# Kernel optimization log

Hardware: AMD Instinct MI355X
Metric: run time of the kernel (lower is better)

The kernel has to match this reference:

```python
import jax, jax.numpy as jnp
import numpy as np

B, N, C, H, E = 16, 512, 128, 8, 131072
Nn = B * N
Dh = C // H
EPS = 1e-5


def setup_inputs() -> dict:
    key = jax.random.key(0)
    ks = jax.random.split(key, 16)
    s = C ** -0.5
    x = jax.random.normal(ks[0], (Nn, C), dtype=jnp.float32)
    edge_index = jax.random.randint(ks[1], (2, E), 0, Nn)
    batch = jnp.arange(Nn) // N  # B equal-sized graphs, sorted
    attn_bias = jax.random.normal(ks[2], (B, N, N, H), dtype=jnp.float32)
    return {
        "x": x,
        "edge_index": edge_index,
        "batch": batch,
        "attn_bias": attn_bias,
        "conv_w": jax.random.normal(ks[3], (C, C)) * s,
        "conv_b": jnp.zeros((C,)),
        "wq": jax.random.normal(ks[4], (C, C)) * s,
        "bq": jnp.zeros((C,)),
        "wk": jax.random.normal(ks[5], (C, C)) * s,
        "bk": jnp.zeros((C,)),
        "wv": jax.random.normal(ks[6], (C, C)) * s,
        "bv": jnp.zeros((C,)),
        "wo": jax.random.normal(ks[7], (C, C)) * s,
        "bo": jnp.zeros((C,)),
        "w1": jax.random.normal(ks[8], (C, 2 * C)) * s,
        "b1": jnp.zeros((2 * C,)),
        "w2": jax.random.normal(ks[9], (2 * C, C)) * (2 * C) ** -0.5,
        "b2": jnp.zeros((C,)),
        "g1": jnp.ones((C,)), "be1": jnp.zeros((C,)),
        "g2": jnp.ones((C,)), "be2": jnp.zeros((C,)),
        "g3": jnp.ones((C,)), "be3": jnp.zeros((C,)),
    }


def _bn(h, g, b):
    # BatchNorm1d over the node dimension (training-mode batch statistics)
    mu = h.mean(axis=0)
    var = h.var(axis=0)  # biased, matches torch normalization
    return g * (h - mu) * jax.lax.rsqrt(var + EPS) + b


def reference(x, edge_index, batch, attn_bias,
              conv_w, conv_b, wq, bq, wk, bk, wv, bv, wo, bo,
              w1, b1, w2, b2, g1, be1, g2, be2, g3, be3):
    n_nodes, ch = x.shape
    bsz, n_max, _, heads = attn_bias.shape
    dh = ch // heads

    # ---- GCN conv (self loops + symmetric norm) -> dropout(0) + residual + norm1
    loops = jnp.arange(n_nodes)
    src = jnp.concatenate([edge_index[0], loops])
    dst = jnp.concatenate([edge_index[1], loops])
    deg = jax.ops.segment_sum(jnp.ones_like(src, dtype=x.dtype), dst, num_segments=n_nodes)
    dinv = jax.lax.rsqrt(jnp.maximum(deg, 1.0))
    xw = x @ conv_w
    msg = xw[src] * (dinv[src] * dinv[dst])[:, None]
    hconv = jax.ops.segment_sum(msg, dst, num_segments=n_nodes) + conv_b
    h1 = _bn(hconv + x, g1, be1)

    # ---- dense batch (equal-sized sorted graphs -> pure reshape, mask all-valid)
    xd = x.reshape(bsz, n_max, ch)
    q = ((xd @ wq + bq) * (dh ** -0.5)).reshape(bsz, n_max, heads, dh)
    k = (xd @ wk + bk).reshape(bsz, n_max, heads, dh)
    v = (xd @ wv + bv).reshape(bsz, n_max, heads, dh)
    scores = jnp.einsum('bqhd,bkhd->bqkh', q, k) + attn_bias  # [B,N,N,H]
    probs = jax.nn.softmax(scores, axis=2)
    att = jnp.einsum('bqkh,bkhd->bqhd', probs, v).reshape(bsz, n_max, ch)
    att = att @ wo + bo
    h2 = _bn(att.reshape(n_nodes, ch) + x, g2, be2)

    # ---- combine branches, MLP with residual, norm3
    out = h1 + h2
    mlp = jax.nn.relu(out @ w1 + b1) @ w2 + b2
    return _bn(out + mlp, g3, be3)
```

## Files before the change

### kernel.cpp

```cpp
#include <hip/hip_runtime.h>
#include <cstddef>

#define NN 8192
#define CC 128

static __device__ inline unsigned f2bf_pack(float a, float b) {
  unsigned ua = __builtin_bit_cast(unsigned, a);
  ua += 0x7fffu + ((ua >> 16) & 1u);
  unsigned ub = __builtin_bit_cast(unsigned, b);
  ub += 0x7fffu + ((ub >> 16) & 1u);
  return (ua >> 16) | (ub & 0xffff0000u);
}
static __device__ inline float bf_lo(unsigned u) { return __builtin_bit_cast(float, u << 16); }
static __device__ inline float bf_hi(unsigned u) { return __builtin_bit_cast(float, u & 0xffff0000u); }

typedef const __attribute__((address_space(1))) void gvoid_t;
typedef __attribute__((address_space(3))) void lvoid_t;
static __device__ inline void glds16(const float* g, float* l) {
  __builtin_amdgcn_global_load_lds((gvoid_t*)g, (lvoid_t*)l, 16, 0, 0);
}


__global__ __launch_bounds__(256) void count_deg_int_k(const int* __restrict__ dst, int* degi, int E) {
  int i = blockIdx.x * 256 + threadIdx.x;
  if (i < E) atomicAdd(&degi[dst[i]], 1);
}

__global__ __launch_bounds__(256) void dinv_k(const int* __restrict__ degi, float* __restrict__ dinv, int n) {
  int i = blockIdx.x * 256 + threadIdx.x;
  if (i < n) dinv[i] = rsqrtf((float)(degi[i] + 1));
}

__global__ __launch_bounds__(256) void scan_k(const int* __restrict__ degi, int* __restrict__ rowstart,
                                              int* __restrict__ cursor) {
  __shared__ int partial[256];
  int t = threadIdx.x;
  int base = t * 32;
  int local[32];
  int s = 0;
#pragma unroll
  for (int i = 0; i < 32; ++i) { local[i] = s; s += degi[base + i]; }
  partial[t] = s;
  __syncthreads();
  for (int off = 1; off < 256; off <<= 1) {
    int v = (t >= off) ? partial[t - off] : 0;
    __syncthreads();
    partial[t] += v;
    __syncthreads();
  }
  int offset = partial[t] - s;
#pragma unroll
  for (int i = 0; i < 32; ++i) {
    rowstart[base + i] = offset + local[i];
    cursor[base + i] = offset + local[i];
  }
  if (t == 255) rowstart[NN] = offset + s;
}

__global__ __launch_bounds__(256) void bucket_k(const int* __restrict__ src, const int* __restrict__ dst,
    int* __restrict__ cursor, int* __restrict__ col, int E) {
  int e = blockIdx.x * 256 + threadIdx.x;
  if (e >= E) return;
  int d = dst[e];
  int pos = atomicAdd(&cursor[d], 1);
  col[pos] = src[e];
}

__global__ __launch_bounds__(256) void gather_k(const int* __restrict__ rowstart, const int* __restrict__ col,
    const float* __restrict__ xws, const float* __restrict__ dinv, const float* __restrict__ cb,
    const float* __restrict__ x, float* __restrict__ h1) {
  int d = blockIdx.x * 2 + (threadIdx.x >> 7);
  int c = threadIdx.x & 127;
  int j0 = rowstart[d], j1 = rowstart[d + 1];
  float dd = dinv[d];
  float sum = 0.f;
  float v = 0.f;
  if (j0 < j1) v = xws[(size_t)col[j0] * CC + c];
  for (int j = j0; j < j1; ++j) {
    float v_next = 0.f;
    if (j + 1 < j1) v_next = xws[(size_t)col[j + 1] * CC + c];
    sum += v;
    v = v_next;
  }
  int idx = d * CC + c;
  sum += xws[idx];
  h1[idx] = sum * dd + cb[c] + x[idx];
}


__global__ __launch_bounds__(256) void bn_stats_k(const float* __restrict__ X,
    float* __restrict__ sums, float* __restrict__ sumsq) {
  int t = threadIdx.x;
  int c = t & 127, rg = t >> 7;
  int r0 = blockIdx.x * 64;
  float s = 0.f, sq = 0.f;
  for (int i = 0; i < 32; ++i) {
    float v = X[(size_t)(r0 + rg + 2 * i) * CC + c];
    s += v; sq += v * v;
  }
  atomicAdd(&sums[c], s);
  atomicAdd(&sumsq[c], sq);
}

__global__ __launch_bounds__(256) void combine_k(const float* __restrict__ h1, const float* __restrict__ h2,
    const float* __restrict__ st, const float* __restrict__ g1, const float* __restrict__ be1,
    const float* __restrict__ g2, const float* __restrict__ be2, float* __restrict__ out) {
  int idx = blockIdx.x * 256 + threadIdx.x;
  int c = idx & 127;
  float mu1 = st[c] * (1.f / NN);
  float var1 = st[128 + c] * (1.f / NN) - mu1 * mu1;
  float sc1 = g1[c] * rsqrtf(var1 + 1e-5f);
  float sh1 = be1[c] - mu1 * sc1;
  float mu2 = st[256 + c] * (1.f / NN);
  float var2 = st[384 + c] * (1.f / NN) - mu2 * mu2;
  float sc2 = g2[c] * rsqrtf(var2 + 1e-5f);
  float sh2 = be2[c] - mu2 * sc2;
  out[idx] = sc1 * h1[idx] + sh1 + sc2 * h2[idx] + sh2;
}

__global__ __launch_bounds__(256) void bn_apply_k(const float* __restrict__ h, const float* __restrict__ st,
    const float* __restrict__ g3, const float* __restrict__ be3, float* __restrict__ out) {
  int idx = blockIdx.x * 256 + threadIdx.x;
  int c = idx & 127;
  float mu = st[512 + c] * (1.f / NN);
  float var = st[640 + c] * (1.f / NN) - mu * mu;
  float sc = g3[c] * rsqrtf(var + 1e-5f);
  float sh = be3[c] - mu * sc;
  out[idx] = sc * h[idx] + sh;
}

__global__ __launch_bounds__(256) void gemm_k(const float* __restrict__ A, const float* __restrict__ W,
    const float* __restrict__ bias, const float* __restrict__ resid, const float* __restrict__ dscale,
    float* __restrict__ out, int M, int N, int K, float scale, int relu) {
  __shared__ float As[64 * 132];
  __shared__ float Ws[128 * 64];
  int t = threadIdx.x;
  int ty = t >> 4, tx = t & 15;
  int row0 = blockIdx.x * 64, n0 = blockIdx.y * 64;
  float acc[4][4] = {};
  for (int kc = 0; kc < K; kc += 128) {
#pragma unroll
    for (int j = 0; j < 8; ++j) {
      int f = t + 256 * j;
      int r = f >> 5, c4 = f & 31;
      *(float4*)(As + r * 132 + c4 * 4) = *(const float4*)(A + (size_t)(row0 + r) * K + kc + c4 * 4);
    }
#pragma unroll
    for (int j = 0; j < 8; ++j) {
      int f = t + 256 * j;
      int kr = f >> 4, c4 = f & 15;
      *(float4*)(Ws + kr * 64 + c4 * 4) = *(const float4*)(W + (size_t)(kc + kr) * N + n0 + c4 * 4);
    }
    __syncthreads();
    for (int k0 = 0; k0 < 128; k0 += 4) {
      float a[4][4], b[4][4];
#pragma unroll
      for (int i = 0; i < 4; ++i) {
        float4 t4 = *(const float4*)(As + (4 * ty + i) * 132 + k0);
        a[i][0] = t4.x; a[i][1] = t4.y; a[i][2] = t4.z; a[i][3] = t4.w;
      }
#pragma unroll
      for (int kk = 0; kk < 4; ++kk) {
        float4 t4 = *(const float4*)(Ws + (k0 + kk) * 64 + 4 * tx);
        b[kk][0] = t4.x; b[kk][1] = t4.y; b[kk][2] = t4.z; b[kk][3] = t4.w;
      }
#pragma unroll
      for (int kk = 0; kk < 4; ++kk)
#pragma unroll
        for (int i = 0; i < 4; ++i)
#pragma unroll
          for (int j = 0; j < 4; ++j)
            acc[i][j] += a[i][kk] * b[kk][j];
    }
    __syncthreads();
  }
  float4 bv = make_float4(0.f, 0.f, 0.f, 0.f);
  if (bias) bv = *(const float4*)(bias + n0 + 4 * tx);
#pragma unroll
  for (int i = 0; i < 4; ++i) {
    int row = row0 + 4 * ty + i;
    float ds = dscale ? dscale[row] : 1.f;
    float4 r;
    r.x = (acc[i][0] + bv.x) * scale * ds;
    r.y = (acc[i][1] + bv.y) * scale * ds;
    r.z = (acc[i][2] + bv.z) * scale * ds;
    r.w = (acc[i][3] + bv.w) * scale * ds;
    if (relu) { r.x = fmaxf(r.x, 0.f); r.y = fmaxf(r.y, 0.f); r.z = fmaxf(r.z, 0.f); r.w = fmaxf(r.w, 0.f); }
    size_t o = (size_t)row * N + n0 + 4 * tx;
    if (resid) {
      float4 rv = *(const float4*)(resid + o);
      r.x += rv.x; r.y += rv.y; r.z += rv.z; r.w += rv.w;
    }
    *(float4*)(out + o) = r;
  }
}

__global__ __launch_bounds__(64, 1) void attn_k(const float* __restrict__ Q, const float* __restrict__ K,
    const float* __restrict__ V, const float* __restrict__ bias,
    unsigned* __restrict__ pA, unsigned* __restrict__ pB, float* __restrict__ lbuf) {
  __shared__ float SM[2][4096];
  const int t = threadIdx.x;
  const int b = blockIdx.x >> 4;
  const int qt = blockIdx.x & 15;
  const int s = blockIdx.y;
  const int qq = t >> 3;
  const int h = t & 7;
  const int node_t = b * 512 + qt * 32;
  const int node0 = node_t + qq * 4;
  const int key0 = s * 128;
  const size_t kvb = ((size_t)b * 512 + key0) * CC;
  const float* bbase = bias + ((size_t)node_t * 512 + key0) * 8;

  float4 qf[4][4];
#pragma unroll
  for (int r = 0; r < 4; ++r)
#pragma unroll
    for (int j = 0; j < 4; ++j)
      qf[r][j] = *(const float4*)(Q + (size_t)(node0 + r) * CC + h * 16 + (((j + h) & 3) << 2));

  float4 acc[4][4];
  float l[4] = {0.f, 0.f, 0.f, 0.f};
#pragma unroll
  for (int r = 0; r < 4; ++r)
#pragma unroll
    for (int j = 0; j < 4; ++j) acc[r][j] = make_float4(0.f, 0.f, 0.f, 0.f);

  auto stage = [&](int ch, int bf) {
    const float* kg = K + kvb + ch * 1024;
    const float* vg = V + kvb + ch * 1024;
    float* ksl = &SM[bf][0];
    float* vsl = &SM[bf][1024];
    float* bsl = &SM[bf][2048];
#pragma unroll
    for (int i = 0; i < 4; ++i) {
      glds16(kg + i * 256 + t * 4, ksl + i * 256);
      glds16(vg + i * 256 + t * 4, vsl + i * 256);
    }
#pragma unroll
    for (int i = 0; i < 8; ++i) {
      int g = i * 64 + t;
      int q = g >> 4;
      int kkp = (g >> 1) & 7;
      int hq = g & 1;
      int kk = (kkp - (q >> 2)) & 7;
      glds16(bbase + (size_t)q * 4096 + (ch * 8 + kk) * 8 + hq * 4, bsl + i * 256);
    }
  };

  stage(0, 0);
  for (int ch = 0; ch < 16; ++ch) {
    int bf = ch & 1;
    if (ch + 1 < 16) stage(ch + 1, bf ^ 1);
    asm volatile("" ::: "memory");
    if (ch + 1 < 16) __builtin_amdgcn_s_waitcnt(0x4F70);
    else             __builtin_amdgcn_s_waitcnt(0x0F70);
    asm volatile("" ::: "memory");
    const float* ksl = &SM[bf][0];
    const float* vsl = &SM[bf][1024];
    const float* bsl = &SM[bf][2048];
#pragma unroll 2
    for (int kk = 0; kk < 8; ++kk) {
      float4 kr[4], vr[4];
#pragma unroll
      for (int j = 0; j < 4; ++j) {
        int off = kk * 128 + h * 16 + (((j + h) & 3) << 2);
        kr[j] = *(const float4*)(ksl + off);
        vr[j] = *(const float4*)(vsl + off);
      }
      int brot = ((kk + qq) & 7) << 3;
#pragma unroll
      for (int r = 0; r < 4; ++r) {
        float sc = bsl[(qq * 4 + r) * 64 + brot + h];
#pragma unroll
        for (int j = 0; j < 4; ++j)
          sc += qf[r][j].x * kr[j].x + qf[r][j].y * kr[j].y
              + qf[r][j].z * kr[j].z + qf[r][j].w * kr[j].w;
        float p = __expf(sc);
        l[r] += p;
#pragma unroll
        for (int j = 0; j < 4; ++j) {
          acc[r][j].x += p * vr[j].x; acc[r][j].y += p * vr[j].y;
          acc[r][j].z += p * vr[j].z; acc[r][j].w += p * vr[j].w;
        }
      }
    }
  }

  unsigned* pbase = (s < 2 ? pA : pB) + (size_t)(s & 1) * (NN * CC / 2);
#pragma unroll
  for (int r = 0; r < 4; ++r) {
    int slot = ((node0 + r) * 8 + h) * 8;
#pragma unroll
    for (int j = 0; j < 4; ++j) {
      int g = (j + h) & 3;
      unsigned u0 = f2bf_pack(acc[r][j].x, acc[r][j].y);
      unsigned u1 = f2bf_pack(acc[r][j].z, acc[r][j].w);
      *(uint2*)(pbase + slot + g * 2) = make_uint2(u0, u1);
    }
    lbuf[s * 65536 + (node0 + r) * 8 + h] = l[r];
  }
}

__global__ __launch_bounds__(256) void attn_merge_k(const unsigned* __restrict__ pA,
    const unsigned* __restrict__ pB, const float* __restrict__ lbuf, float* __restrict__ out) {
  int i = blockIdx.x * 256 + threadIdx.x;
  float L = lbuf[i] + lbuf[65536 + i] + lbuf[131072 + i] + lbuf[196608 + i];
  float inv = 1.f / L;
  float o[16];
#pragma unroll
  for (int d = 0; d < 16; ++d) o[d] = 0.f;
#pragma unroll
  for (int s = 0; s < 4; ++s) {
    const unsigned* pb = (s < 2 ? pA : pB) + (size_t)(s & 1) * (NN * CC / 2) + (size_t)i * 8;
    uint4 a = *(const uint4*)pb;
    uint4 b = *(const uint4*)(pb + 4);
    unsigned u[8] = {a.x, a.y, a.z, a.w, b.x, b.y, b.z, b.w};
#pragma unroll
    for (int j = 0; j < 8; ++j) {
      o[2*j]   += bf_lo(u[j]);
      o[2*j+1] += bf_hi(u[j]);
    }
  }
  float* po = out + (size_t)i * 16;
#pragma unroll
  for (int j = 0; j < 4; ++j)
    *(float4*)(po + 4 * j) = make_float4(o[4*j] * inv, o[4*j+1] * inv, o[4*j+2] * inv, o[4*j+3] * inv);
}


extern "C" void kernel_launch(void* const* d_in, const int* in_sizes, int n_in,
                              void* d_out, int out_size, void* d_ws, size_t ws_size,
                              hipStream_t stream) {
  const float* x      = (const float*)d_in[0];
  const int*   ei     = (const int*)d_in[1];
  const float* bias   = (const float*)d_in[3];
  const float* conv_w = (const float*)d_in[4];
  const float* conv_b = (const float*)d_in[5];
  const float* wq = (const float*)d_in[6];
  const float* bq = (const float*)d_in[7];
  const float* wk = (const float*)d_in[8];
  const float* bk = (const float*)d_in[9];
  const float* wv = (const float*)d_in[10];
  const float* bv = (const float*)d_in[11];
  const float* wo = (const float*)d_in[12];
  const float* bo = (const float*)d_in[13];
  const float* w1 = (const float*)d_in[14];
  const float* b1 = (const float*)d_in[15];
  const float* w2 = (const float*)d_in[16];
  const float* b2 = (const float*)d_in[17];
  const float* g1 = (const float*)d_in[18];
  const float* be1 = (const float*)d_in[19];
  const float* g2 = (const float*)d_in[20];
  const float* be2 = (const float*)d_in[21];
  const float* g3 = (const float*)d_in[22];
  const float* be3 = (const float*)d_in[23];
  int E = in_sizes[1] / 2;

  float* ws = (float*)d_ws;
  const size_t NC = (size_t)NN * CC;
  float* xw     = ws;
  float* h1pre  = ws + NC;
  float* qb     = ws + 2 * NC;
  float* kb     = ws + 3 * NC;
  float* vb     = ws + 4 * NC;
  float* h2pre  = ws + 5 * NC;
  float* outbuf = ws + 6 * NC;
  float* hid    = ws + 2 * NC;
  float* h3pre  = ws + 4 * NC;
  float* st     = ws + 7 * NC;
  float* dinv   = ws + 7 * NC + 768;
  int*   degi     = (int*)(ws + 7 * NC + 768 + NN);
  int*   rowstart = degi + NN;
  int*   cursor   = rowstart + NN + 1;
  int*   col      = cursor + NN;
  float* lbuf     = (float*)(col + E);

  hipMemsetAsync(degi, 0, NN * sizeof(int), stream);
  hipMemsetAsync(st, 0, 768 * sizeof(float), stream);

  count_deg_int_k<<<(E + 255) / 256, 256, 0, stream>>>(ei + E, degi, E);
  dinv_k<<<NN / 256, 256, 0, stream>>>(degi, dinv, NN);
  scan_k<<<1, 256, 0, stream>>>(degi, rowstart, cursor);
  bucket_k<<<(E + 255) / 256, 256, 0, stream>>>(ei, ei + E, cursor, col, E);
  gemm_k<<<dim3(NN / 64, 2), 256, 0, stream>>>(x, conv_w, nullptr, nullptr, dinv, xw, NN, CC, CC, 1.f, 0);
  gather_k<<<NN / 2, 256, 0, stream>>>(rowstart, col, xw, dinv, conv_b, x, h1pre);
  bn_stats_k<<<NN / 64, 256, 0, stream>>>(h1pre, st + 0, st + 128);

  gemm_k<<<dim3(NN / 64, 2), 256, 0, stream>>>(x, wq, bq, nullptr, nullptr, qb, NN, CC, CC, 0.25f, 0);
  gemm_k<<<dim3(NN / 64, 2), 256, 0, stream>>>(x, wk, bk, nullptr, nullptr, kb, NN, CC, CC, 1.f, 0);
  gemm_k<<<dim3(NN / 64, 2), 256, 0, stream>>>(x, wv, bv, nullptr, nullptr, vb, NN, CC, CC, 1.f, 0);
  attn_k<<<dim3(256, 4), 64, 0, stream>>>(qb, kb, vb, bias, (unsigned*)xw, (unsigned*)h2pre, lbuf);
  attn_merge_k<<<65536 / 256, 256, 0, stream>>>((unsigned*)xw, (unsigned*)h2pre, lbuf, outbuf);
  gemm_k<<<dim3(NN / 64, 2), 256, 0, stream>>>(outbuf, wo, bo, x, nullptr, h2pre, NN, CC, CC, 1.f, 0);
  bn_stats_k<<<NN / 64, 256, 0, stream>>>(h2pre, st + 256, st + 384);

  combine_k<<<NC / 256, 256, 0, stream>>>(h1pre, h2pre, st, g1, be1, g2, be2, outbuf);
  gemm_k<<<dim3(NN / 64, 4), 256, 0, stream>>>(outbuf, w1, b1, nullptr, nullptr, hid, NN, 2 * CC, CC, 1.f, 1);
  gemm_k<<<dim3(NN / 64, 2), 256, 0, stream>>>(hid, w2, b2, outbuf, nullptr, h3pre, NN, CC, 2 * CC, 1.f, 0);
  bn_stats_k<<<NN / 64, 256, 0, stream>>>(h3pre, st + 512, st + 640);
  bn_apply_k<<<NC / 256, 256, 0, stream>>>(h3pre, st, g3, be3, (float*)d_out);
}
```

Baseline: 440.7 us.

## Shrink attention blocks to one query row per thread for more occupancy

```diff
diff --git a/kernel.cpp b/kernel.cpp
--- a/kernel.cpp
+++ b/kernel.cpp
@@ -195,71 +195,66 @@
   }
 }
 
-__global__ __launch_bounds__(64, 1) void attn_k(const float* __restrict__ Q, const float* __restrict__ K,
+__global__ __launch_bounds__(64, 4) void attn_k(const float* __restrict__ Q, const float* __restrict__ K,
     const float* __restrict__ V, const float* __restrict__ bias,
     unsigned* __restrict__ pA, unsigned* __restrict__ pB, float* __restrict__ lbuf) {
-  __shared__ float SM[2][4096];
+  __shared__ float SM[2][1280];
   const int t = threadIdx.x;
-  const int b = blockIdx.x >> 4;
-  const int qt = blockIdx.x & 15;
-  const int s = blockIdx.y;
-  const int qq = t >> 3;
+  const int orig = blockIdx.x;
+  const int lb = ((orig & 7) << 9) | (orig >> 3);
+  const int grp = lb >> 6;
+  const int qt = lb & 63;
+  const int b = grp >> 2;
+  const int s = grp & 3;
+  const int q = t >> 3;
   const int h = t & 7;
-  const int node_t = b * 512 + qt * 32;
-  const int node0 = node_t + qq * 4;
+  const int node_t = b * 512 + qt * 8;
+  const int node = node_t + q;
   const int key0 = s * 128;
   const size_t kvb = ((size_t)b * 512 + key0) * CC;
   const float* bbase = bias + ((size_t)node_t * 512 + key0) * 8;
 
-  float4 qf[4][4];
-#pragma unroll
-  for (int r = 0; r < 4; ++r)
-#pragma unroll
-    for (int j = 0; j < 4; ++j)
-      qf[r][j] = *(const float4*)(Q + (size_t)(node0 + r) * CC + h * 16 + (((j + h) & 3) << 2));
-
-  float4 acc[4][4];
-  float l[4] = {0.f, 0.f, 0.f, 0.f};
-#pragma unroll
-  for (int r = 0; r < 4; ++r)
-#pragma unroll
-    for (int j = 0; j < 4; ++j) acc[r][j] = make_float4(0.f, 0.f, 0.f, 0.f);
+  float4 qf[4];
+#pragma unroll
+  for (int j = 0; j < 4; ++j)
+    qf[j] = *(const float4*)(Q + (size_t)node * CC + h * 16 + (((j + h) & 3) << 2));
+
+  float4 acc[4];
+  float lsum = 0.f;
+#pragma unroll
+  for (int j = 0; j < 4; ++j) acc[j] = make_float4(0.f, 0.f, 0.f, 0.f);
 
   auto stage = [&](int ch, int bf) {
-    const float* kg = K + kvb + ch * 1024;
-    const float* vg = V + kvb + ch * 1024;
+    const float* kg = K + kvb + ch * 512;
+    const float* vg = V + kvb + ch * 512;
     float* ksl = &SM[bf][0];
-    float* vsl = &SM[bf][1024];
-    float* bsl = &SM[bf][2048];
-#pragma unroll
-    for (int i = 0; i < 4; ++i) {
+    float* vsl = &SM[bf][512];
+    float* bsl = &SM[bf][1024];
+#pragma unroll
+    for (int i = 0; i < 2; ++i) {
       glds16(kg + i * 256 + t * 4, ksl + i * 256);
       glds16(vg + i * 256 + t * 4, vsl + i * 256);
     }
-#pragma unroll
-    for (int i = 0; i < 8; ++i) {
-      int g = i * 64 + t;
-      int q = g >> 4;
-      int kkp = (g >> 1) & 7;
-      int hq = g & 1;
-      int kk = (kkp - (q >> 2)) & 7;
-      glds16(bbase + (size_t)q * 4096 + (ch * 8 + kk) * 8 + hq * 4, bsl + i * 256);
+    {
+      int ql = t >> 3, kkp = (t >> 1) & 3, hq = t & 1;
+      int kks = (kkp - ql) & 3;
+      glds16(bbase + (size_t)ql * 4096 + (size_t)(ch * 4 + kks) * 8 + hq * 4, bsl);
     }
   };
 
   stage(0, 0);
-  for (int ch = 0; ch < 16; ++ch) {
+  for (int ch = 0; ch < 32; ++ch) {
     int bf = ch & 1;
-    if (ch + 1 < 16) stage(ch + 1, bf ^ 1);
+    if (ch + 1 < 32) stage(ch + 1, bf ^ 1);
     asm volatile("" ::: "memory");
-    if (ch + 1 < 16) __builtin_amdgcn_s_waitcnt(0x4F70);
+    if (ch + 1 < 32) __builtin_amdgcn_s_waitcnt(0x0F75);
     else             __builtin_amdgcn_s_waitcnt(0x0F70);
     asm volatile("" ::: "memory");
     const float* ksl = &SM[bf][0];
-    const float* vsl = &SM[bf][1024];
-    const float* bsl = &SM[bf][2048];
-#pragma unroll 2
-    for (int kk = 0; kk < 8; ++kk) {
+    const float* vsl = &SM[bf][512];
+    const float* bsl = &SM[bf][1024];
+#pragma unroll
+    for (int kk = 0; kk < 4; ++kk) {
       float4 kr[4], vr[4];
 #pragma unroll
       for (int j = 0; j < 4; ++j) {
@@ -267,38 +262,33 @@
         kr[j] = *(const float4*)(ksl + off);
         vr[j] = *(const float4*)(vsl + off);
       }
-      int brot = ((kk + qq) & 7) << 3;
-#pragma unroll
-      for (int r = 0; r < 4; ++r) {
-        float sc = bsl[(qq * 4 + r) * 64 + brot + h];
-#pragma unroll
-        for (int j = 0; j < 4; ++j)
-          sc += qf[r][j].x * kr[j].x + qf[r][j].y * kr[j].y
-              + qf[r][j].z * kr[j].z + qf[r][j].w * kr[j].w;
-        float p = __expf(sc);
-        l[r] += p;
-#pragma unroll
-        for (int j = 0; j < 4; ++j) {
-          acc[r][j].x += p * vr[j].x; acc[r][j].y += p * vr[j].y;
-          acc[r][j].z += p * vr[j].z; acc[r][j].w += p * vr[j].w;
-        }
+      float sc = bsl[q * 32 + (((kk + q) & 3) << 3) + h];
+#pragma unroll
+      for (int j = 0; j < 4; ++j)
+        sc += qf[j].x * kr[j].x + qf[j].y * kr[j].y
+            + qf[j].z * kr[j].z + qf[j].w * kr[j].w;
+      float p = __expf(sc);
+      lsum += p;
+#pragma unroll
+      for (int j = 0; j < 4; ++j) {
+        acc[j].x += p * vr[j].x; acc[j].y += p * vr[j].y;
+        acc[j].z += p * vr[j].z; acc[j].w += p * vr[j].w;
       }
     }
   }
 
   unsigned* pbase = (s < 2 ? pA : pB) + (size_t)(s & 1) * (NN * CC / 2);
-#pragma unroll
-  for (int r = 0; r < 4; ++r) {
-    int slot = ((node0 + r) * 8 + h) * 8;
-#pragma unroll
-    for (int j = 0; j < 4; ++j) {
-      int g = (j + h) & 3;
-      unsigned u0 = f2bf_pack(acc[r][j].x, acc[r][j].y);
-      unsigned u1 = f2bf_pack(acc[r][j].z, acc[r][j].w);
-      *(uint2*)(pbase + slot + g * 2) = make_uint2(u0, u1);
-    }
-    lbuf[s * 65536 + (node0 + r) * 8 + h] = l[r];
-  }
+  int slot = (node * 8 + h) * 8;
+  unsigned u[8];
+#pragma unroll
+  for (int g = 0; g < 4; ++g) {
+    int j = (g - h) & 3;
+    u[2 * g]     = f2bf_pack(acc[j].x, acc[j].y);
+    u[2 * g + 1] = f2bf_pack(acc[j].z, acc[j].w);
+  }
+  *(uint4*)(pbase + slot)     = make_uint4(u[0], u[1], u[2], u[3]);
+  *(uint4*)(pbase + slot + 4) = make_uint4(u[4], u[5], u[6], u[7]);
+  lbuf[s * 65536 + node * 8 + h] = lsum;
 }
 
 __global__ __launch_bounds__(256) void attn_merge_k(const unsigned* __restrict__ pA,
@@ -389,7 +379,7 @@
   gemm_k<<<dim3(NN / 64, 2), 256, 0, stream>>>(x, wq, bq, nullptr, nullptr, qb, NN, CC, CC, 0.25f, 0);
   gemm_k<<<dim3(NN / 64, 2), 256, 0, stream>>>(x, wk, bk, nullptr, nullptr, kb, NN, CC, CC, 1.f, 0);
   gemm_k<<<dim3(NN / 64, 2), 256, 0, stream>>>(x, wv, bv, nullptr, nullptr, vb, NN, CC, CC, 1.f, 0);
-  attn_k<<<dim3(256, 4), 64, 0, stream>>>(qb, kb, vb, bias, (unsigned*)xw, (unsigned*)h2pre, lbuf);
+  attn_k<<<4096, 64, 0, stream>>>(qb, kb, vb, bias, (unsigned*)xw, (unsigned*)h2pre, lbuf);
   attn_merge_k<<<65536 / 256, 256, 0, stream>>>((unsigned*)xw, (unsigned*)h2pre, lbuf, outbuf);
   gemm_k<<<dim3(NN / 64, 2), 256, 0, stream>>>(outbuf, wo, bo, x, nullptr, h2pre, NN, CC, CC, 1.f, 0);
   bn_stats_k<<<NN / 64, 256, 0, stream>>>(h2pre, st + 256, st + 384);
```

Result: no change. 446.2 us (+1.2%).

## Split attention keys into eight chunks and interleave query rows per thread

Applied to the files above, without the earlier changes.

```diff
diff --git a/kernel.cpp b/kernel.cpp
--- a/kernel.cpp
+++ b/kernel.cpp
@@ -195,19 +195,21 @@
   }
 }
 
-__global__ __launch_bounds__(64, 1) void attn_k(const float* __restrict__ Q, const float* __restrict__ K,
+__global__ __launch_bounds__(64, 2) void attn_k(const float* __restrict__ Q, const float* __restrict__ K,
     const float* __restrict__ V, const float* __restrict__ bias,
-    unsigned* __restrict__ pA, unsigned* __restrict__ pB, float* __restrict__ lbuf) {
-  __shared__ float SM[2][4096];
+    unsigned* __restrict__ p0, unsigned* __restrict__ p1,
+    unsigned* __restrict__ p2, unsigned* __restrict__ p3, float* __restrict__ lbuf) {
+  __shared__ float SM[2][2048];
   const int t = threadIdx.x;
-  const int b = blockIdx.x >> 4;
-  const int qt = blockIdx.x & 15;
-  const int s = blockIdx.y;
+  const int orig = blockIdx.x;
+  const int s = orig & 7;
+  const int qtg = orig >> 3;
+  const int b = qtg >> 4;
+  const int qt = qtg & 15;
   const int qq = t >> 3;
   const int h = t & 7;
   const int node_t = b * 512 + qt * 32;
-  const int node0 = node_t + qq * 4;
-  const int key0 = s * 128;
+  const int key0 = s * 64;
   const size_t kvb = ((size_t)b * 512 + key0) * CC;
   const float* bbase = bias + ((size_t)node_t * 512 + key0) * 8;
 
@@ -216,7 +218,7 @@
   for (int r = 0; r < 4; ++r)
 #pragma unroll
     for (int j = 0; j < 4; ++j)
-      qf[r][j] = *(const float4*)(Q + (size_t)(node0 + r) * CC + h * 16 + (((j + h) & 3) << 2));
+      qf[r][j] = *(const float4*)(Q + (size_t)(node_t + qq + 8 * r) * CC + h * 16 + (((j + h) & 3) << 2));
 
   float4 acc[4][4];
   float l[4] = {0.f, 0.f, 0.f, 0.f};
@@ -226,24 +228,23 @@
     for (int j = 0; j < 4; ++j) acc[r][j] = make_float4(0.f, 0.f, 0.f, 0.f);
 
   auto stage = [&](int ch, int bf) {
-    const float* kg = K + kvb + ch * 1024;
-    const float* vg = V + kvb + ch * 1024;
+    const float* kg = K + kvb + ch * 512;
+    const float* vg = V + kvb + ch * 512;
     float* ksl = &SM[bf][0];
-    float* vsl = &SM[bf][1024];
-    float* bsl = &SM[bf][2048];
-#pragma unroll
-    for (int i = 0; i < 4; ++i) {
+    float* vsl = &SM[bf][512];
+    float* bsl = &SM[bf][1024];
+#pragma unroll
+    for (int i = 0; i < 2; ++i) {
       glds16(kg + i * 256 + t * 4, ksl + i * 256);
       glds16(vg + i * 256 + t * 4, vsl + i * 256);
     }
 #pragma unroll
-    for (int i = 0; i < 8; ++i) {
-      int g = i * 64 + t;
-      int q = g >> 4;
-      int kkp = (g >> 1) & 7;
-      int hq = g & 1;
-      int kk = (kkp - (q >> 2)) & 7;
-      glds16(bbase + (size_t)q * 4096 + (ch * 8 + kk) * 8 + hq * 4, bsl + i * 256);
+    for (int i = 0; i < 4; ++i) {
+      int q = i * 8 + (t >> 3);
+      int kkp = (t >> 1) & 3;
+      int hq = t & 1;
+      int kks = (kkp - q) & 3;
+      glds16(bbase + (size_t)q * 4096 + (size_t)(ch * 4 + kks) * 8 + hq * 4, bsl + i * 256);
     }
   };
 
@@ -252,14 +253,14 @@
     int bf = ch & 1;
     if (ch + 1 < 16) stage(ch + 1, bf ^ 1);
     asm volatile("" ::: "memory");
-    if (ch + 1 < 16) __builtin_amdgcn_s_waitcnt(0x4F70);
+    if (ch + 1 < 16) __builtin_amdgcn_s_waitcnt(0x0F78);
     else             __builtin_amdgcn_s_waitcnt(0x0F70);
     asm volatile("" ::: "memory");
     const float* ksl = &SM[bf][0];
-    const float* vsl = &SM[bf][1024];
-    const float* bsl = &SM[bf][2048];
-#pragma unroll 2
-    for (int kk = 0; kk < 8; ++kk) {
+    const float* vsl = &SM[bf][512];
+    const float* bsl = &SM[bf][1024];
+#pragma unroll
+    for (int kk = 0; kk < 4; ++kk) {
       float4 kr[4], vr[4];
 #pragma unroll
       for (int j = 0; j < 4; ++j) {
@@ -267,10 +268,10 @@
         kr[j] = *(const float4*)(ksl + off);
         vr[j] = *(const float4*)(vsl + off);
       }
-      int brot = ((kk + qq) & 7) << 3;
+      int brot = ((kk + qq) & 3) << 3;
 #pragma unroll
       for (int r = 0; r < 4; ++r) {
-        float sc = bsl[(qq * 4 + r) * 64 + brot + h];
+        float sc = bsl[qq * 32 + r * 256 + brot + h];
 #pragma unroll
         for (int j = 0; j < 4; ++j)
           sc += qf[r][j].x * kr[j].x + qf[r][j].y * kr[j].y
@@ -286,32 +287,40 @@
     }
   }
 
-  unsigned* pbase = (s < 2 ? pA : pB) + (size_t)(s & 1) * (NN * CC / 2);
+  unsigned* preg = (s < 4) ? ((s < 2) ? p0 : p1) : ((s < 6) ? p2 : p3);
+  unsigned* pbase = preg + (size_t)(s & 1) * (NN * CC / 2);
 #pragma unroll
   for (int r = 0; r < 4; ++r) {
-    int slot = ((node0 + r) * 8 + h) * 8;
-#pragma unroll
-    for (int j = 0; j < 4; ++j) {
-      int g = (j + h) & 3;
-      unsigned u0 = f2bf_pack(acc[r][j].x, acc[r][j].y);
-      unsigned u1 = f2bf_pack(acc[r][j].z, acc[r][j].w);
-      *(uint2*)(pbase + slot + g * 2) = make_uint2(u0, u1);
-    }
-    lbuf[s * 65536 + (node0 + r) * 8 + h] = l[r];
-  }
-}
-
-__global__ __launch_bounds__(256) void attn_merge_k(const unsigned* __restrict__ pA,
-    const unsigned* __restrict__ pB, const float* __restrict__ lbuf, float* __restrict__ out) {
+    int node = node_t + qq + 8 * r;
+    int slot = (node * 8 + h) * 8;
+    unsigned u[8];
+#pragma unroll
+    for (int g = 0; g < 4; ++g) {
+      int j = (g - h) & 3;
+      u[2 * g]     = f2bf_pack(acc[r][j].x, acc[r][j].y);
+      u[2 * g + 1] = f2bf_pack(acc[r][j].z, acc[r][j].w);
+    }
+    *(uint4*)(pbase + slot)     = make_uint4(u[0], u[1], u[2], u[3]);
+    *(uint4*)(pbase + slot + 4) = make_uint4(u[4], u[5], u[6], u[7]);
+    lbuf[s * 65536 + node * 8 + h] = l[r];
+  }
+}
+
+__global__ __launch_bounds__(256) void attn_merge_k(const unsigned* __restrict__ p0,
+    const unsigned* __restrict__ p1, const unsigned* __restrict__ p2, const unsigned* __restrict__ p3,
+    const float* __restrict__ lbuf, float* __restrict__ out) {
   int i = blockIdx.x * 256 + threadIdx.x;
-  float L = lbuf[i] + lbuf[65536 + i] + lbuf[131072 + i] + lbuf[196608 + i];
+  float L = 0.f;
+#pragma unroll
+  for (int s = 0; s < 8; ++s) L += lbuf[s * 65536 + i];
   float inv = 1.f / L;
   float o[16];
 #pragma unroll
   for (int d = 0; d < 16; ++d) o[d] = 0.f;
-#pragma unroll
-  for (int s = 0; s < 4; ++s) {
-    const unsigned* pb = (s < 2 ? pA : pB) + (size_t)(s & 1) * (NN * CC / 2) + (size_t)i * 8;
+  const unsigned* regs[4] = {p0, p1, p2, p3};
+#pragma unroll
+  for (int s = 0; s < 8; ++s) {
+    const unsigned* pb = regs[s >> 1] + (size_t)(s & 1) * (NN * CC / 2) + (size_t)i * 8;
     uint4 a = *(const uint4*)pb;
     uint4 b = *(const uint4*)(pb + 4);
     unsigned u[8] = {a.x, a.y, a.z, a.w, b.x, b.y, b.z, b.w};
@@ -389,9 +398,11 @@
   gemm_k<<<dim3(NN / 64, 2), 256, 0, stream>>>(x, wq, bq, nullptr, nullptr, qb, NN, CC, CC, 0.25f, 0);
   gemm_k<<<dim3(NN / 64, 2), 256, 0, stream>>>(x, wk, bk, nullptr, nullptr, kb, NN, CC, CC, 1.f, 0);
   gemm_k<<<dim3(NN / 64, 2), 256, 0, stream>>>(x, wv, bv, nullptr, nullptr, vb, NN, CC, CC, 1.f, 0);
-  attn_k<<<dim3(256, 4), 64, 0, stream>>>(qb, kb, vb, bias, (unsigned*)xw, (unsigned*)h2pre, lbuf);
-  attn_merge_k<<<65536 / 256, 256, 0, stream>>>((unsigned*)xw, (unsigned*)h2pre, lbuf, outbuf);
-  gemm_k<<<dim3(NN / 64, 2), 256, 0, stream>>>(outbuf, wo, bo, x, nullptr, h2pre, NN, CC, CC, 1.f, 0);
+  attn_k<<<2048, 64, 0, stream>>>(qb, kb, vb, bias,
+      (unsigned*)xw, (unsigned*)h2pre, (unsigned*)d_out, (unsigned*)outbuf, lbuf);
+  attn_merge_k<<<65536 / 256, 256, 0, stream>>>((unsigned*)xw, (unsigned*)h2pre,
+      (unsigned*)d_out, (unsigned*)outbuf, lbuf, vb);
+  gemm_k<<<dim3(NN / 64, 2), 256, 0, stream>>>(vb, wo, bo, x, nullptr, h2pre, NN, CC, CC, 1.f, 0);
   bn_stats_k<<<NN / 64, 256, 0, stream>>>(h2pre, st + 256, st + 384);
 
   combine_k<<<NC / 256, 256, 0, stream>>>(h1pre, h2pre, st, g1, be1, g2, be2, outbuf);
```

Result: slower. 474.6 us (+7.7%).
